# Kernel optimization log

Measured on AMD Instinct MI355X. Metric: run time of the kernel, lower is better.

Reference implementation:

```python
import jax, jax.numpy as jnp
import numpy as np

L, B, D, H = 512, 128, 512, 1024  # length, batch, input_dim, hidden


def setup_inputs() -> dict:
    key = jax.random.key(0)
    ks = jax.random.split(key, 5)
    s_in = 1.0 / np.sqrt(D + H)
    return {
        "x": jax.random.normal(ks[0], (L, B, D), dtype=jnp.float32),
        "h0": jax.random.normal(ks[1], (B, H), dtype=jnp.float32),
        "W_z": jax.random.normal(ks[2], (H, D + H), dtype=jnp.float32) * s_in,
        "b_z": jnp.zeros((H,), dtype=jnp.float32),
        "W_r": jax.random.normal(ks[3], (H, D + H), dtype=jnp.float32) * s_in,
        "b_r": jnp.zeros((H,), dtype=jnp.float32),
        "W_h": jax.random.normal(ks[4], (H, D + H), dtype=jnp.float32) * s_in,
        "b_h": jnp.zeros((H,), dtype=jnp.float32),
    }


def reference(x, h0, W_z, b_z, W_r, b_r, W_h, b_h):
    # GRU recurrence: gates computed from concat([h, x]) as in the torch code.
    def step(h, x_t):
        hx = jnp.concatenate([h, x_t], axis=-1)            # [B, H+D]
        z = jax.nn.sigmoid(hx @ W_z.T + b_z)               # update gate
        r = jax.nn.sigmoid(hx @ W_r.T + b_r)               # reset gate
        rhx = jnp.concatenate([r * h, x_t], axis=-1)       # [B, H+D]
        h_tilde = jnp.tanh(rhx @ W_h.T + b_h)
        h_new = (1.0 - z) * h + z * h_tilde
        return h_new, h_new

    _, outputs = jax.lax.scan(step, h0, x)  # outputs: [L, B, H]
    return outputs
```

## Files before the change

kernel.cpp:

```cpp
#include <hip/hip_runtime.h>
#include <cstdint>
#include <cstddef>

#define LT 512
#define BB 128
#define DD 512
#define HH 1024
#define HD 1536
#define MT (LT*BB)

typedef __bf16 bf16;
typedef __bf16 bf16x8 __attribute__((ext_vector_type(8)));
typedef __bf16 bf16x4 __attribute__((ext_vector_type(4)));
typedef float  f32x4  __attribute__((ext_vector_type(4)));

#define O_WZR 0u
#define O_WHR 6291456u
#define O_WXH 8388608u
#define O_XB  9437184u
#define O_HB  76546048u
#define O_RHB 76808192u
#define O_ZB  77070336u
#define O_BAR 77594624u
#define O_FLG 77660160u
#define WS_NEED 77922304u

#define WAIT_VM0() asm volatile("s_waitcnt vmcnt(0)" ::: "memory")
#define SCHED0()   __builtin_amdgcn_sched_barrier(0)
#define L1_INV()   asm volatile("buffer_inv sc0" ::: "memory")

template<int L> __device__ __forceinline__ f32x4 ld16s(const void* p) {
  f32x4 r;
  if constexpr (L) asm volatile("global_load_dwordx4 %0, %1, off sc0"     : "=&v"(r) : "v"(p) : "memory");
  else             asm volatile("global_load_dwordx4 %0, %1, off sc0 sc1" : "=&v"(r) : "v"(p) : "memory");
  return r;
}
template<int L> __device__ __forceinline__ float ld4s(const void* p) {
  float r;
  if constexpr (L) asm volatile("global_load_dword %0, %1, off sc0"     : "=&v"(r) : "v"(p) : "memory");
  else             asm volatile("global_load_dword %0, %1, off sc0 sc1" : "=&v"(r) : "v"(p) : "memory");
  return r;
}
template<int L> __device__ __forceinline__ unsigned ld2s(const void* p) {
  unsigned r;
  if constexpr (L) asm volatile("global_load_ushort %0, %1, off sc0"     : "=&v"(r) : "v"(p) : "memory");
  else             asm volatile("global_load_ushort %0, %1, off sc0 sc1" : "=&v"(r) : "v"(p) : "memory");
  return r;
}
template<int L> __device__ __forceinline__ void st4s(float* p, float v) {
  if constexpr (L) asm volatile("global_store_dword %0, %1, off sc0"     :: "v"(p), "v"(v) : "memory");
  else             asm volatile("global_store_dword %0, %1, off sc0 sc1" :: "v"(p), "v"(v) : "memory");
}
template<int L> __device__ __forceinline__ void st2s(bf16* p, unsigned v) {
  if constexpr (L) asm volatile("global_store_short %0, %1, off sc0"     :: "v"(p), "v"(v) : "memory");
  else             asm volatile("global_store_short %0, %1, off sc0 sc1" :: "v"(p), "v"(v) : "memory");
}
__device__ __forceinline__ void st_flag(unsigned char* p, unsigned v) {
  asm volatile("global_store_byte %0, %1, off sc0" :: "v"(p), "v"(v) : "memory");
}
__device__ __forceinline__ unsigned ld_flag(const unsigned char* p) {
  unsigned r;
  asm volatile("global_load_ubyte %0, %1, off sc0\n\ts_waitcnt vmcnt(0)"
               : "=&v"(r) : "v"(p) : "memory");
  return r;
}
__device__ __forceinline__ unsigned bf16_bits(float f) {
  bf16 b = (bf16)f;
  return (unsigned)__builtin_bit_cast(unsigned short, b);
}
__device__ __forceinline__ float bits_to_f32(unsigned u16) {
  return __builtin_bit_cast(float, u16 << 16);
}

__device__ __forceinline__ void bar_sync(unsigned* cntA, unsigned char* flagst,
                                         int t, int voteok, int& use_local,
                                         unsigned tgtA, int tid, int lane, int wv, int sb) {
  WAIT_VM0();
  __syncthreads();
  if (tid == 0)
    __hip_atomic_fetch_add(cntA, 1u, __ATOMIC_RELAXED, __HIP_MEMORY_SCOPE_AGENT);
  if (wv == 0) {
    if (tid == 0 && voteok) st_flag(flagst + sb, 1u);
    int done = 0;
    if (use_local && t >= 2) {
      int gd = 1500;
      while (gd--) {
        L1_INV();
        unsigned ok = 1u;
        if (lane < 32) ok = ld_flag(flagst + lane);
        if (__ballot(ok != 0u) == ~0ull) { done = 1; break; }
      }
      if (!done) use_local = 0;
    }
    if (!done && tid == 0) {
      int gd = 60000;
      while (__hip_atomic_load(cntA, __ATOMIC_RELAXED, __HIP_MEMORY_SCOPE_AGENT) < tgtA
             && --gd) __builtin_amdgcn_s_sleep(2);
    }
    L1_INV();
  }
  __syncthreads();
}

__global__ void k_cvt(const float* __restrict__ s, bf16* __restrict__ d, int n8) {
  int i = blockIdx.x*256 + threadIdx.x;
  if (i >= n8) return;
  const float4* p = (const float4*)s + (size_t)i*2;
  float4 a = p[0], b = p[1];
  bf16x8 v = {(bf16)a.x,(bf16)a.y,(bf16)a.z,(bf16)a.w,(bf16)b.x,(bf16)b.y,(bf16)b.z,(bf16)b.w};
  *((bf16x8*)d + i) = v;
}

__global__ void k_split_wh(const float* __restrict__ Wh, bf16* __restrict__ whr, bf16* __restrict__ wxh) {
  int i = blockIdx.x*256 + threadIdx.x;
  if (i >= 1024*192) return;
  int row = i / 192, c8 = (i % 192)*8;
  const float4* p = (const float4*)(Wh + (size_t)row*HD + c8);
  float4 a = p[0], b = p[1];
  bf16x8 v = {(bf16)a.x,(bf16)a.y,(bf16)a.z,(bf16)a.w,(bf16)b.x,(bf16)b.y,(bf16)b.z,(bf16)b.w};
  bf16* dptr = (c8 < HH) ? (whr + (size_t)row*HH + c8) : (wxh + (size_t)row*DD + (c8 - HH));
  *(bf16x8*)dptr = v;
}

__global__ void k_init_h(const float* __restrict__ h0, bf16* __restrict__ hb) {
  int i = blockIdx.x*256 + threadIdx.x;
  float4 a = ((const float4*)h0)[i];
  bf16x4 v = {(bf16)a.x,(bf16)a.y,(bf16)a.z,(bf16)a.w};
  *((bf16x4*)hb + i) = v;
}

__global__ __launch_bounds__(256) void k_gemm_xh(
    const bf16* __restrict__ xb, const bf16* __restrict__ wxh,
    const float* __restrict__ bh, float* __restrict__ out)
{
  __shared__ char As[16384];
  __shared__ char Bs[16384];
  const int bid = blockIdx.x;
  const int nt8 = bid & 7, mtb = bid >> 3;
  const int tid = threadIdx.x;
  const int lane = tid & 63, wv = tid >> 6;
  const int l15 = lane & 15, q = lane >> 4;
  const int wm = wv >> 1, wn = wv & 1;
  f32x4 acc[4][4] = {};
  const char* Ab = (const char*)(xb + (size_t)mtb*128*DD);
  const char* Bb = (const char*)(wxh + (size_t)nt8*128*DD);
  const int crow = tid >> 3, ccb = (tid & 7)*16;
  const int cdst = crow*128 + (ccb ^ ((crow & 7) << 4));
  for (int kt = 0; kt < 8; ++kt) {
    __syncthreads();
    #pragma unroll
    for (int i = 0; i < 4; ++i) {
      *(uint4*)(As + cdst + i*4096) = *(const uint4*)(Ab + (size_t)(crow + i*32)*1024 + kt*128 + ccb);
      *(uint4*)(Bs + cdst + i*4096) = *(const uint4*)(Bb + (size_t)(crow + i*32)*1024 + kt*128 + ccb);
    }
    __syncthreads();
    #pragma unroll
    for (int ks = 0; ks < 2; ++ks) {
      bf16x8 af[4], bfr[4];
      #pragma unroll
      for (int m4 = 0; m4 < 4; ++m4) {
        int row = wm*64 + m4*16 + l15, cb = ks*64 + 16*q;
        af[m4] = *(const bf16x8*)(As + row*128 + (cb ^ ((row&7)<<4)));
      }
      #pragma unroll
      for (int n4 = 0; n4 < 4; ++n4) {
        int row = wn*64 + n4*16 + l15, cb = ks*64 + 16*q;
        bfr[n4] = *(const bf16x8*)(Bs + row*128 + (cb ^ ((row&7)<<4)));
      }
      #pragma unroll
      for (int m4 = 0; m4 < 4; ++m4)
        #pragma unroll
        for (int n4 = 0; n4 < 4; ++n4)
          acc[m4][n4] = __builtin_amdgcn_mfma_f32_16x16x32_bf16(af[m4], bfr[n4], acc[m4][n4], 0, 0, 0);
    }
  }
  const int jb = nt8*128 + wn*64;
  const size_t mb = (size_t)mtb*128 + wm*64;
  #pragma unroll
  for (int n4 = 0; n4 < 4; ++n4) {
    int j = jb + n4*16 + l15;
    float bias = bh[j];
    #pragma unroll
    for (int m4 = 0; m4 < 4; ++m4)
      #pragma unroll
      for (int e = 0; e < 4; ++e) {
        size_t m = mb + m4*16 + 4*q + e;
        out[m*HH + j] = acc[m4][n4][e] + bias;
      }
  }
}

struct Frags { bf16x8 zr[4][2]; bf16x8 h[8]; };

template<int L>
__device__ __forceinline__ void tloop(const Frags& F, char* ldsW, char* scr,
    const bf16* __restrict__ xb, float* __restrict__ out,
    bf16* __restrict__ hb, bf16* __restrict__ rhb, float* __restrict__ zbuf,
    unsigned* cnt1A, unsigned* cnt2A, unsigned char* flg1, unsigned char* flg2,
    int voteok, int g, int sb, int ch, int kh, int tid, int lane, int wv,
    const float (&bias)[2], float (&hreg)[4])
{
  const int l15 = lane & 15, q = lane >> 4;
  const bf16* hrow = hb  + (size_t)(g*16 + l15)*HH;
  const bf16* rrow = rhb + (size_t)(g*16 + l15)*HH;
  const int kh384 = kh*384, kh256 = kh*256;
  const int jown = sb*32 + ch*16 + l15;
  int use_local = L ? voteok : 0;

  for (int t = 0; t < LT; ++t) {
    {
      f32x4 ab[12];
      const bf16* xrow = xb + (size_t)(t*BB + g*16 + l15)*DD;
      #pragma unroll
      for (int kk = 0; kk < 12; ++kk) {
        int kabs = kh384 + kk*32;
        if (kabs < HH) ab[kk] = ld16s<L>(hrow + kabs + 8*q);
        else           ab[kk] = *(const f32x4*)(xrow + (kabs - HH) + 8*q);
      }
      unsigned hv[2][4];
      if (sb >= 16 && kh == 0) {
        #pragma unroll
        for (int nt = 0; nt < 2; ++nt) {
          int cr = sb*64 - HH + ch*32 + nt*16 + l15;
          #pragma unroll
          for (int e = 0; e < 4; ++e)
            hv[nt][e] = ld2s<L>(hb + (size_t)(g*16 + 4*q + e)*HH + cr);
        }
      }
      WAIT_VM0(); SCHED0();
      f32x4 a0 = {}, a1 = {};
      #pragma unroll
      for (int kk = 0; kk < 12; ++kk) {
        bf16x8 a = __builtin_bit_cast(bf16x8, ab[kk]);
        bf16x8 b0, b1;
        if (kk < 8) {
          b0 = *(const bf16x8*)(ldsW + (ch*32      + l15)*2064 + kh*512 + kk*64 + 16*q);
          b1 = *(const bf16x8*)(ldsW + (ch*32 + 16 + l15)*2064 + kh*512 + kk*64 + 16*q);
        } else { b0 = F.zr[kk-8][0]; b1 = F.zr[kk-8][1]; }
        a0 = __builtin_amdgcn_mfma_f32_16x16x32_bf16(a, b0, a0, 0, 0, 0);
        a1 = __builtin_amdgcn_mfma_f32_16x16x32_bf16(a, b1, a1, 0, 0, 0);
      }
      if (kh) {
        int s = ((kh-1)*2 + ch)*2;
        *(f32x4*)(scr + (s+0)*1024 + lane*16) = a0;
        *(f32x4*)(scr + (s+1)*1024 + lane*16) = a1;
      }
      __syncthreads();
      if (kh == 0) {
        #pragma unroll
        for (int k2 = 0; k2 < 3; ++k2) {
          int s = (k2*2 + ch)*2;
          a0 += *(const f32x4*)(scr + (s+0)*1024 + lane*16);
          a1 += *(const f32x4*)(scr + (s+1)*1024 + lane*16);
        }
        if (sb < 16) {
          #pragma unroll
          for (int nt = 0; nt < 2; ++nt) {
            f32x4 ac = nt ? a1 : a0;
            int c = sb*64 + ch*32 + nt*16 + l15;
            #pragma unroll
            for (int e = 0; e < 4; ++e) {
              int m = g*16 + 4*q + e;
              float gate = 1.f/(1.f + __expf(-(ac[e] + bias[nt])));
              st4s<L>(zbuf + (size_t)m*HH + c, gate);
            }
          }
        } else {
          #pragma unroll
          for (int nt = 0; nt < 2; ++nt) {
            f32x4 ac = nt ? a1 : a0;
            int cr = sb*64 - HH + ch*32 + nt*16 + l15;
            #pragma unroll
            for (int e = 0; e < 4; ++e) {
              int m = g*16 + 4*q + e;
              float gate = 1.f/(1.f + __expf(-(ac[e] + bias[nt])));
              st2s<L>(rhb + (size_t)m*HH + cr, bf16_bits(gate * bits_to_f32(hv[nt][e])));
            }
          }
        }
      }
    }
    bar_sync(cnt1A, flg1 + t*32, t, L ? voteok : 0, use_local,
             32u*(unsigned)(t+1), tid, lane, wv, sb);
    {
      f32x4 rb[8];
      #pragma unroll
      for (int kk = 0; kk < 8; ++kk)
        rb[kk] = ld16s<L>(rrow + kh256 + kk*32 + 8*q);
      float zv[4], xh[4];
      if (kh == 0) {
        #pragma unroll
        for (int e = 0; e < 4; ++e) {
          int m = g*16 + 4*q + e;
          zv[e] = ld4s<L>(zbuf + (size_t)m*HH + jown);
          xh[e] = out[(size_t)t*(BB*HH) + (size_t)m*HH + jown];
        }
      }
      WAIT_VM0(); SCHED0();
      f32x4 acc = {};
      #pragma unroll
      for (int kk = 0; kk < 8; ++kk)
        acc = __builtin_amdgcn_mfma_f32_16x16x32_bf16(
            __builtin_bit_cast(bf16x8, rb[kk]), F.h[kk], acc, 0, 0, 0);
      if (kh) *(f32x4*)(scr + ((kh-1)*2 + ch)*1024 + lane*16) = acc;
      __syncthreads();
      if (kh == 0) {
        #pragma unroll
        for (int k2 = 0; k2 < 3; ++k2)
          acc += *(const f32x4*)(scr + (k2*2 + ch)*1024 + lane*16);
        #pragma unroll
        for (int e = 0; e < 4; ++e) {
          int m = g*16 + 4*q + e;
          size_t idx = (size_t)m*HH + jown;
          size_t oidx = (size_t)t*(BB*HH) + idx;
          float ht = tanhf(acc[e] + xh[e]);
          float hn = hreg[e] + zv[e]*(ht - hreg[e]);
          out[oidx] = hn;
          hreg[e] = hn;
          st2s<L>(hb + idx, bf16_bits(hn));
        }
      }
    }
    bar_sync(cnt2A, flg2 + t*32, t, L ? voteok : 0, use_local,
             32u*(unsigned)(t+1), tid, lane, wv, sb);
    if (L && tid == 0 && voteok && t + 2 < LT) {
      st_flag(flg1 + (t+2)*32 + sb, 0u);
      st_flag(flg2 + (t+2)*32 + sb, 0u);
    }
  }
}

__global__ __launch_bounds__(512) void k_gru(
    const bf16* __restrict__ Wzr, const bf16* __restrict__ Whr,
    const bf16* __restrict__ xb, const float* __restrict__ h0,
    const float* __restrict__ bz, const float* __restrict__ br,
    float* __restrict__ out,
    bf16* __restrict__ hb, bf16* __restrict__ rhb, float* __restrict__ zbuf,
    unsigned* __restrict__ bar, unsigned char* __restrict__ flg)
{
  extern __shared__ char smem[];
  char* ldsW = smem;
  char* scr  = smem + 132096;
  volatile int* modep = (volatile int*)(smem + 144384);

  const int tid = threadIdx.x, bid = blockIdx.x;
  const int lane = tid & 63, wv = tid >> 6;
  const int l15 = lane & 15, q = lane >> 4;
  const int g = bid & 7, sb = bid >> 3;
  const int ch = wv & 1, kh = wv >> 1;
  unsigned* grp   = bar + (size_t)g*2048;
  unsigned* cnt1A = grp + 40;
  unsigned* cnt2A = grp + 48;
  unsigned char* flg1 = flg + (size_t)g*32768;
  unsigned char* flg2 = flg + (size_t)g*32768 + 16384;

  #pragma unroll
  for (int i = 0; i < 16; ++i) {
    int ci = tid + i*512;
    int row = ci >> 7, c = ci & 127;
    int le = c*8, khs = le >> 8, rem = le & 255;
    *(uint4*)(ldsW + row*2064 + c*16) =
      *(const uint4*)(Wzr + (size_t)(sb*64 + row)*HD + khs*384 + rem);
  }
  Frags F;
  #pragma unroll
  for (int i = 0; i < 4; ++i)
    #pragma unroll
    for (int nt = 0; nt < 2; ++nt)
      F.zr[i][nt] = *(const bf16x8*)(Wzr + (size_t)(sb*64 + ch*32 + nt*16 + l15)*HD
                                     + kh*384 + (8+i)*32 + 8*q);
  #pragma unroll
  for (int kk = 0; kk < 8; ++kk)
    F.h[kk] = *(const bf16x8*)(Whr + (size_t)(sb*32 + ch*16 + l15)*HH + kh*256 + kk*32 + 8*q);

  float bias[2];
  #pragma unroll
  for (int nt = 0; nt < 2; ++nt) {
    int c = sb*64 + ch*32 + nt*16 + l15;
    bias[nt] = (sb < 16) ? bz[c] : br[c - HH];
  }
  float hreg[4];
  const int jown = sb*32 + ch*16 + l15;
  #pragma unroll
  for (int e = 0; e < 4; ++e)
    hreg[e] = h0[(size_t)(g*16 + 4*q + e)*HH + jown];

  if (tid == 0) {
    int xcc;
    asm("s_getreg_b32 %0, hwreg(HW_REG_XCC_ID)" : "=s"(xcc));
    __hip_atomic_store(&grp[sb], (unsigned)(xcc + 1), __ATOMIC_RELAXED, __HIP_MEMORY_SCOPE_AGENT);
    unsigned first = 0; int ok = 1;
    long budget = 200000;
    for (int i = 0; i < 32; ++i) {
      unsigned v = 0;
      while (budget > 0) {
        v = __hip_atomic_load(&grp[i], __ATOMIC_RELAXED, __HIP_MEMORY_SCOPE_AGENT);
        if (v) break;
        --budget; __builtin_amdgcn_s_sleep(8);
      }
      if (!v) { ok = 0; break; }
      if (i == 0) first = v;
      else if (v != first) { ok = 0; break; }
    }
    *modep = ok;
  }
  __syncthreads();
  int voteok = *modep;

  if (voteok) tloop<1>(F, ldsW, scr, xb, out, hb, rhb, zbuf, cnt1A, cnt2A,
                       flg1, flg2, 1, g, sb, ch, kh, tid, lane, wv, bias, hreg);
  else        tloop<0>(F, ldsW, scr, xb, out, hb, rhb, zbuf, cnt1A, cnt2A,
                       flg1, flg2, 0, g, sb, ch, kh, tid, lane, wv, bias, hreg);
}

extern "C" void kernel_launch(void* const* d_in, const int* in_sizes, int n_in,
                              void* d_out, int out_size, void* d_ws, size_t ws_size,
                              hipStream_t stream) {
  const float* x  = (const float*)d_in[0];
  const float* h0 = (const float*)d_in[1];
  const float* Wz = (const float*)d_in[2];
  const float* bz = (const float*)d_in[3];
  const float* Wr = (const float*)d_in[4];
  const float* br = (const float*)d_in[5];
  const float* Wh = (const float*)d_in[6];
  const float* bh = (const float*)d_in[7];
  float* out = (float*)d_out;
  char* ws = (char*)d_ws;
  if (ws_size < (size_t)WS_NEED) return;

  bf16*  wzr  = (bf16*) (ws + O_WZR);
  bf16*  whr  = (bf16*) (ws + O_WHR);
  bf16*  wxh  = (bf16*) (ws + O_WXH);
  bf16*  xbb  = (bf16*) (ws + O_XB);
  bf16*  hb   = (bf16*) (ws + O_HB);
  bf16*  rhb  = (bf16*) (ws + O_RHB);
  float* zbuf = (float*)(ws + O_ZB);
  unsigned* bar = (unsigned*)(ws + O_BAR);
  unsigned char* flg = (unsigned char*)(ws + O_FLG);

  hipMemsetAsync(bar, 0, 65536, stream);
  k_cvt<<<16384, 256, 0, stream>>>(x, xbb, MT*DD/8);
  k_cvt<<<768, 256, 0, stream>>>(Wz, wzr, HH*HD/8);
  k_cvt<<<768, 256, 0, stream>>>(Wr, wzr + (size_t)HH*HD, HH*HD/8);
  k_split_wh<<<768, 256, 0, stream>>>(Wh, whr, wxh);
  k_init_h<<<128, 256, 0, stream>>>(h0, hb);
  k_gemm_xh<<<4096, 256, 0, stream>>>(xbb, wxh, bh, out);

  hipFuncSetAttribute((const void*)k_gru, hipFuncAttributeMaxDynamicSharedMemorySize, 144400);
  k_gru<<<256, 512, 144400, stream>>>(wzr, whr, xbb, h0, bz, br, out, hb, rhb, zbuf, bar, flg);
}
```

Measured before the change: 5.241 ms.

## Streamline grid barrier to single-wave signaling and prefetch next-step x and out

Removes the full-block bar_sync, which waited on all memory ops and ran two __syncthreads. Only the kh==0 waves now store results, and a wave-to-wave LDS handshake lets a single wave do the cross-block atomic and flag polling before one __syncthreads. The x operand for step t+1 is prefetched during the second phase, and the xh loads from out are moved earlier so they overlap the first GEMM, with partial vmcnt waits. Risks include subtle ordering bugs in the LDS spin handshake and extra register pressure from keeping ab live across iterations. Launch bounds also change to (512,2).

After: 6.155 ms. 17.4% more time.

```diff
diff --git a/kernel.cpp b/kernel.cpp
--- a/kernel.cpp
+++ b/kernel.cpp
@@ -25,9 +25,11 @@
 #define O_FLG 77660160u
 #define WS_NEED 77922304u
 
-#define WAIT_VM0() asm volatile("s_waitcnt vmcnt(0)" ::: "memory")
-#define SCHED0()   __builtin_amdgcn_sched_barrier(0)
-#define L1_INV()   asm volatile("buffer_inv sc0" ::: "memory")
+#define WAIT_VM0()  asm volatile("s_waitcnt vmcnt(0)" ::: "memory")
+#define WAIT_VM4()  asm volatile("s_waitcnt vmcnt(4)" ::: "memory")
+#define WAIT_VM12() asm volatile("s_waitcnt vmcnt(12)" ::: "memory")
+#define SCHED0()    __builtin_amdgcn_sched_barrier(0)
+#define L1_INV()    asm volatile("buffer_inv sc0" ::: "memory")
 
 template<int L> __device__ __forceinline__ f32x4 ld16s(const void* p) {
   f32x4 r;
@@ -55,6 +57,16 @@
   if constexpr (L) asm volatile("global_store_short %0, %1, off sc0"     :: "v"(p), "v"(v) : "memory");
   else             asm volatile("global_store_short %0, %1, off sc0 sc1" :: "v"(p), "v"(v) : "memory");
 }
+__device__ __forceinline__ f32x4 ld16p(const void* p) {
+  f32x4 r;
+  asm volatile("global_load_dwordx4 %0, %1, off" : "=&v"(r) : "v"(p) : "memory");
+  return r;
+}
+__device__ __forceinline__ float ld4p(const void* p) {
+  float r;
+  asm volatile("global_load_dword %0, %1, off" : "=&v"(r) : "v"(p) : "memory");
+  return r;
+}
 __device__ __forceinline__ void st_flag(unsigned char* p, unsigned v) {
   asm volatile("global_store_byte %0, %1, off sc0" :: "v"(p), "v"(v) : "memory");
 }
@@ -70,36 +82,6 @@
 }
 __device__ __forceinline__ float bits_to_f32(unsigned u16) {
   return __builtin_bit_cast(float, u16 << 16);
-}
-
-__device__ __forceinline__ void bar_sync(unsigned* cntA, unsigned char* flagst,
-                                         int t, int voteok, int& use_local,
-                                         unsigned tgtA, int tid, int lane, int wv, int sb) {
-  WAIT_VM0();
-  __syncthreads();
-  if (tid == 0)
-    __hip_atomic_fetch_add(cntA, 1u, __ATOMIC_RELAXED, __HIP_MEMORY_SCOPE_AGENT);
-  if (wv == 0) {
-    if (tid == 0 && voteok) st_flag(flagst + sb, 1u);
-    int done = 0;
-    if (use_local && t >= 2) {
-      int gd = 1500;
-      while (gd--) {
-        L1_INV();
-        unsigned ok = 1u;
-        if (lane < 32) ok = ld_flag(flagst + lane);
-        if (__ballot(ok != 0u) == ~0ull) { done = 1; break; }
-      }
-      if (!done) use_local = 0;
-    }
-    if (!done && tid == 0) {
-      int gd = 60000;
-      while (__hip_atomic_load(cntA, __ATOMIC_RELAXED, __HIP_MEMORY_SCOPE_AGENT) < tgtA
-             && --gd) __builtin_amdgcn_s_sleep(2);
-    }
-    L1_INV();
-  }
-  __syncthreads();
 }
 
 __global__ void k_cvt(const float* __restrict__ s, bf16* __restrict__ d, int n8) {
@@ -200,22 +182,32 @@
     int voteok, int g, int sb, int ch, int kh, int tid, int lane, int wv,
     const float (&bias)[2], float (&hreg)[4])
 {
+  __shared__ unsigned s_done[2];
   const int l15 = lane & 15, q = lane >> 4;
   const bf16* hrow = hb  + (size_t)(g*16 + l15)*HH;
   const bf16* rrow = rhb + (size_t)(g*16 + l15)*HH;
   const int kh384 = kh*384, kh256 = kh*256;
   const int jown = sb*32 + ch*16 + l15;
   int use_local = L ? voteok : 0;
+  if (tid == 0) { s_done[0] = 0; s_done[1] = 0; }
+
+  f32x4 ab[12];
+  {
+    const bf16* xrow0 = xb + (size_t)(g*16 + l15)*DD;
+    #pragma unroll
+    for (int kk = 0; kk < 12; ++kk) {
+      int kabs = kh384 + kk*32;
+      if (kabs >= HH) ab[kk] = ld16p(xrow0 + (kabs - HH) + 8*q);
+    }
+  }
 
   for (int t = 0; t < LT; ++t) {
+    float xh[4];
     {
-      f32x4 ab[12];
-      const bf16* xrow = xb + (size_t)(t*BB + g*16 + l15)*DD;
       #pragma unroll
       for (int kk = 0; kk < 12; ++kk) {
         int kabs = kh384 + kk*32;
         if (kabs < HH) ab[kk] = ld16s<L>(hrow + kabs + 8*q);
-        else           ab[kk] = *(const f32x4*)(xrow + (kabs - HH) + 8*q);
       }
       unsigned hv[2][4];
       if (sb >= 16 && kh == 0) {
@@ -227,7 +219,13 @@
             hv[nt][e] = ld2s<L>(hb + (size_t)(g*16 + 4*q + e)*HH + cr);
         }
       }
-      WAIT_VM0(); SCHED0();
+      if (kh == 0) {
+        #pragma unroll
+        for (int e = 0; e < 4; ++e)
+          xh[e] = ld4p(out + (size_t)t*(BB*HH) + (size_t)(g*16 + 4*q + e)*HH + jown);
+      }
+      if (kh == 0) { WAIT_VM4(); } else { WAIT_VM0(); }
+      SCHED0();
       f32x4 a0 = {}, a1 = {};
       #pragma unroll
       for (int kk = 0; kk < 12; ++kk) {
@@ -278,25 +276,65 @@
             }
           }
         }
-      }
+        WAIT_VM0();
+        if (ch == 1) {
+          if (lane == 0)
+            __hip_atomic_fetch_add(&s_done[0], 1u, __ATOMIC_RELAXED, __HIP_MEMORY_SCOPE_WORKGROUP);
+        } else {
+          if (lane == 0) {
+            int gd = 1<<22;
+            while (!__hip_atomic_load(&s_done[0], __ATOMIC_RELAXED, __HIP_MEMORY_SCOPE_WORKGROUP) && --gd) {}
+            __hip_atomic_store(&s_done[0], 0u, __ATOMIC_RELAXED, __HIP_MEMORY_SCOPE_WORKGROUP);
+            __hip_atomic_fetch_add(cnt1A, 1u, __ATOMIC_RELAXED, __HIP_MEMORY_SCOPE_AGENT);
+            if (L && voteok) st_flag(flg1 + t*32 + sb, 1u);
+          }
+          int done = 0;
+          if (use_local && t >= 2) {
+            int gd = 1500;
+            while (gd--) {
+              L1_INV();
+              unsigned ok = 1u;
+              if (lane < 32) ok = ld_flag(flg1 + t*32 + lane);
+              if (__ballot(ok != 0u) == ~0ull) { done = 1; break; }
+            }
+            if (!done) use_local = 0;
+          }
+          if (!done && lane == 0) {
+            unsigned tgt = 32u*(unsigned)(t+1);
+            int gd = 60000;
+            while (__hip_atomic_load(cnt1A, __ATOMIC_RELAXED, __HIP_MEMORY_SCOPE_AGENT) < tgt
+                   && --gd) __builtin_amdgcn_s_sleep(2);
+          }
+          L1_INV();
+        }
+      }
+      __syncthreads();
     }
-    bar_sync(cnt1A, flg1 + t*32, t, L ? voteok : 0, use_local,
-             32u*(unsigned)(t+1), tid, lane, wv, sb);
     {
       f32x4 rb[8];
       #pragma unroll
       for (int kk = 0; kk < 8; ++kk)
         rb[kk] = ld16s<L>(rrow + kh256 + kk*32 + 8*q);
-      float zv[4], xh[4];
+      float zv[4];
       if (kh == 0) {
         #pragma unroll
-        for (int e = 0; e < 4; ++e) {
-          int m = g*16 + 4*q + e;
-          zv[e] = ld4s<L>(zbuf + (size_t)m*HH + jown);
-          xh[e] = out[(size_t)t*(BB*HH) + (size_t)m*HH + jown];
-        }
-      }
-      WAIT_VM0(); SCHED0();
+        for (int e = 0; e < 4; ++e)
+          zv[e] = ld4s<L>(zbuf + (size_t)(g*16 + 4*q + e)*HH + jown);
+      }
+      {
+        int tn = (t+1 < LT) ? t+1 : t;
+        const bf16* xrow_n = xb + (size_t)(tn*BB + g*16 + l15)*DD;
+        #pragma unroll
+        for (int kk = 0; kk < 12; ++kk) {
+          int kabs = kh384 + kk*32;
+          if (kabs >= HH) ab[kk] = ld16p(xrow_n + (kabs - HH) + 8*q);
+        }
+      }
+      if      (kh == 3) { WAIT_VM12(); }
+      else if (kh == 2) { WAIT_VM4(); }
+      else if (kh == 0) { WAIT_VM4(); }
+      else              { WAIT_VM0(); }
+      SCHED0();
       f32x4 acc = {};
       #pragma unroll
       for (int kk = 0; kk < 8; ++kk)
@@ -305,6 +343,7 @@
       if (kh) *(f32x4*)(scr + ((kh-1)*2 + ch)*1024 + lane*16) = acc;
       __syncthreads();
       if (kh == 0) {
+        WAIT_VM0(); SCHED0();
         #pragma unroll
         for (int k2 = 0; k2 < 3; ++k2)
           acc += *(const f32x4*)(scr + (k2*2 + ch)*1024 + lane*16);
@@ -319,18 +358,48 @@
           hreg[e] = hn;
           st2s<L>(hb + idx, bf16_bits(hn));
         }
+        WAIT_VM0();
+        if (ch == 1) {
+          if (lane == 0)
+            __hip_atomic_fetch_add(&s_done[1], 1u, __ATOMIC_RELAXED, __HIP_MEMORY_SCOPE_WORKGROUP);
+        } else {
+          if (lane == 0) {
+            int gd = 1<<22;
+            while (!__hip_atomic_load(&s_done[1], __ATOMIC_RELAXED, __HIP_MEMORY_SCOPE_WORKGROUP) && --gd) {}
+            __hip_atomic_store(&s_done[1], 0u, __ATOMIC_RELAXED, __HIP_MEMORY_SCOPE_WORKGROUP);
+            __hip_atomic_fetch_add(cnt2A, 1u, __ATOMIC_RELAXED, __HIP_MEMORY_SCOPE_AGENT);
+            if (L && voteok) st_flag(flg2 + t*32 + sb, 1u);
+          }
+          int done = 0;
+          if (use_local && t >= 2) {
+            int gd = 1500;
+            while (gd--) {
+              L1_INV();
+              unsigned ok = 1u;
+              if (lane < 32) ok = ld_flag(flg2 + t*32 + lane);
+              if (__ballot(ok != 0u) == ~0ull) { done = 1; break; }
+            }
+            if (!done) use_local = 0;
+          }
+          if (!done && lane == 0) {
+            unsigned tgt = 32u*(unsigned)(t+1);
+            int gd = 60000;
+            while (__hip_atomic_load(cnt2A, __ATOMIC_RELAXED, __HIP_MEMORY_SCOPE_AGENT) < tgt
+                   && --gd) __builtin_amdgcn_s_sleep(2);
+          }
+          L1_INV();
+        }
+      }
+      __syncthreads();
+      if (L && tid == 0 && voteok && t + 2 < LT) {
+        st_flag(flg1 + (t+2)*32 + sb, 0u);
+        st_flag(flg2 + (t+2)*32 + sb, 0u);
       }
     }
-    bar_sync(cnt2A, flg2 + t*32, t, L ? voteok : 0, use_local,
-             32u*(unsigned)(t+1), tid, lane, wv, sb);
-    if (L && tid == 0 && voteok && t + 2 < LT) {
-      st_flag(flg1 + (t+2)*32 + sb, 0u);
-      st_flag(flg2 + (t+2)*32 + sb, 0u);
-    }
-  }
-}
-
-__global__ __launch_bounds__(512) void k_gru(
+  }
+}
+
+__global__ __launch_bounds__(512, 2) void k_gru(
     const bf16* __restrict__ Wzr, const bf16* __restrict__ Whr,
     const bf16* __restrict__ xb, const float* __restrict__ h0,
     const float* __restrict__ bz, const float* __restrict__ br,
@@ -341,7 +410,7 @@
   extern __shared__ char smem[];
   char* ldsW = smem;
   char* scr  = smem + 132096;
-  volatile int* modep = (volatile int*)(smem + 144384);
+  __shared__ int s_mode;
 
   const int tid = threadIdx.x, bid = blockIdx.x;
   const int lane = tid & 63, wv = tid >> 6;
@@ -402,10 +471,10 @@
       if (i == 0) first = v;
       else if (v != first) { ok = 0; break; }
     }
-    *modep = ok;
+    s_mode = ok;
   }
   __syncthreads();
-  int voteok = *modep;
+  int voteok = s_mode;
 
   if (voteok) tloop<1>(F, ldsW, scr, xb, out, hb, rhb, zbuf, cnt1A, cnt2A,
                        flg1, flg2, 1, g, sb, ch, kh, tid, lane, wv, bias, hreg);
@@ -446,6 +515,6 @@
   k_init_h<<<128, 256, 0, stream>>>(h0, hb);
   k_gemm_xh<<<4096, 256, 0, stream>>>(xbb, wxh, bh, out);
 
-  hipFuncSetAttribute((const void*)k_gru, hipFuncAttributeMaxDynamicSharedMemorySize, 144400);
-  k_gru<<<256, 512, 144400, stream>>>(wzr, whr, xbb, h0, bz, br, out, hb, rhb, zbuf, bar, flg);
-}
+  hipFuncSetAttribute((const void*)k_gru, hipFuncAttributeMaxDynamicSharedMemorySize, 144384);
+  k_gru<<<256, 512, 144384, stream>>>(wzr, whr, xbb, h0, bz, br, out, hb, rhb, zbuf, bar, flg);
+}
```

## Co-locate z and r gate columns per block to keep z gate in LDS

Applied to the files above, without the earlier changes.

Each block used to compute 64 columns that were either all z-gate or all r-gate, so the z gate went out to a global buffer and was read back after the grid barrier. Now each block computes the 32 z columns and the 32 r columns that match its own hidden slice. The z values stay in shared memory and are read by the same block in phase two. This removes a global store and a global load per step on the serial critical path, at the cost of a little more LDS and a changed weight-row mapping.

Result: faster. 4.616 ms (-11.9%).

```diff
diff --git a/kernel.cpp b/kernel.cpp
--- a/kernel.cpp
+++ b/kernel.cpp
@@ -20,7 +20,6 @@
 #define O_XB  9437184u
 #define O_HB  76546048u
 #define O_RHB 76808192u
-#define O_ZB  77070336u
 #define O_BAR 77594624u
 #define O_FLG 77660160u
 #define WS_NEED 77922304u
@@ -35,21 +34,11 @@
   else             asm volatile("global_load_dwordx4 %0, %1, off sc0 sc1" : "=&v"(r) : "v"(p) : "memory");
   return r;
 }
-template<int L> __device__ __forceinline__ float ld4s(const void* p) {
-  float r;
-  if constexpr (L) asm volatile("global_load_dword %0, %1, off sc0"     : "=&v"(r) : "v"(p) : "memory");
-  else             asm volatile("global_load_dword %0, %1, off sc0 sc1" : "=&v"(r) : "v"(p) : "memory");
-  return r;
-}
 template<int L> __device__ __forceinline__ unsigned ld2s(const void* p) {
   unsigned r;
   if constexpr (L) asm volatile("global_load_ushort %0, %1, off sc0"     : "=&v"(r) : "v"(p) : "memory");
   else             asm volatile("global_load_ushort %0, %1, off sc0 sc1" : "=&v"(r) : "v"(p) : "memory");
   return r;
-}
-template<int L> __device__ __forceinline__ void st4s(float* p, float v) {
-  if constexpr (L) asm volatile("global_store_dword %0, %1, off sc0"     :: "v"(p), "v"(v) : "memory");
-  else             asm volatile("global_store_dword %0, %1, off sc0 sc1" :: "v"(p), "v"(v) : "memory");
 }
 template<int L> __device__ __forceinline__ void st2s(bf16* p, unsigned v) {
   if constexpr (L) asm volatile("global_store_short %0, %1, off sc0"     :: "v"(p), "v"(v) : "memory");
@@ -193,9 +182,9 @@
 struct Frags { bf16x8 zr[4][2]; bf16x8 h[8]; };
 
 template<int L>
-__device__ __forceinline__ void tloop(const Frags& F, char* ldsW, char* scr,
+__device__ __forceinline__ void tloop(const Frags& F, char* ldsW, char* scr, float* zsL,
     const bf16* __restrict__ xb, float* __restrict__ out,
-    bf16* __restrict__ hb, bf16* __restrict__ rhb, float* __restrict__ zbuf,
+    bf16* __restrict__ hb, bf16* __restrict__ rhb,
     unsigned* cnt1A, unsigned* cnt2A, unsigned char* flg1, unsigned char* flg2,
     int voteok, int g, int sb, int ch, int kh, int tid, int lane, int wv,
     const float (&bias)[2], float (&hreg)[4])
@@ -218,10 +207,10 @@
         else           ab[kk] = *(const f32x4*)(xrow + (kabs - HH) + 8*q);
       }
       unsigned hv[2][4];
-      if (sb >= 16 && kh == 0) {
+      if (ch == 1 && kh == 0) {
         #pragma unroll
         for (int nt = 0; nt < 2; ++nt) {
-          int cr = sb*64 - HH + ch*32 + nt*16 + l15;
+          int cr = sb*32 + nt*16 + l15;
           #pragma unroll
           for (int e = 0; e < 4; ++e)
             hv[nt][e] = ld2s<L>(hb + (size_t)(g*16 + 4*q + e)*HH + cr);
@@ -253,23 +242,20 @@
           a0 += *(const f32x4*)(scr + (s+0)*1024 + lane*16);
           a1 += *(const f32x4*)(scr + (s+1)*1024 + lane*16);
         }
-        if (sb < 16) {
+        if (ch == 0) {
           #pragma unroll
           for (int nt = 0; nt < 2; ++nt) {
             f32x4 ac = nt ? a1 : a0;
-            int c = sb*64 + ch*32 + nt*16 + l15;
             #pragma unroll
-            for (int e = 0; e < 4; ++e) {
-              int m = g*16 + 4*q + e;
-              float gate = 1.f/(1.f + __expf(-(ac[e] + bias[nt])));
-              st4s<L>(zbuf + (size_t)m*HH + c, gate);
-            }
+            for (int e = 0; e < 4; ++e)
+              zsL[(nt*16 + l15)*16 + 4*q + e] =
+                1.f/(1.f + __expf(-(ac[e] + bias[nt])));
           }
         } else {
           #pragma unroll
           for (int nt = 0; nt < 2; ++nt) {
             f32x4 ac = nt ? a1 : a0;
-            int cr = sb*64 - HH + ch*32 + nt*16 + l15;
+            int cr = sb*32 + nt*16 + l15;
             #pragma unroll
             for (int e = 0; e < 4; ++e) {
               int m = g*16 + 4*q + e;
@@ -287,14 +273,11 @@
       #pragma unroll
       for (int kk = 0; kk < 8; ++kk)
         rb[kk] = ld16s<L>(rrow + kh256 + kk*32 + 8*q);
-      float zv[4], xh[4];
+      float xh[4];
       if (kh == 0) {
         #pragma unroll
-        for (int e = 0; e < 4; ++e) {
-          int m = g*16 + 4*q + e;
-          zv[e] = ld4s<L>(zbuf + (size_t)m*HH + jown);
-          xh[e] = out[(size_t)t*(BB*HH) + (size_t)m*HH + jown];
-        }
+        for (int e = 0; e < 4; ++e)
+          xh[e] = out[(size_t)t*(BB*HH) + (size_t)(g*16 + 4*q + e)*HH + jown];
       }
       WAIT_VM0(); SCHED0();
       f32x4 acc = {};
@@ -308,6 +291,7 @@
         #pragma unroll
         for (int k2 = 0; k2 < 3; ++k2)
           acc += *(const f32x4*)(scr + (k2*2 + ch)*1024 + lane*16);
+        f32x4 zv = *(const f32x4*)(zsL + (ch*16 + l15)*16 + 4*q);
         #pragma unroll
         for (int e = 0; e < 4; ++e) {
           int m = g*16 + 4*q + e;
@@ -335,13 +319,14 @@
     const bf16* __restrict__ xb, const float* __restrict__ h0,
     const float* __restrict__ bz, const float* __restrict__ br,
     float* __restrict__ out,
-    bf16* __restrict__ hb, bf16* __restrict__ rhb, float* __restrict__ zbuf,
+    bf16* __restrict__ hb, bf16* __restrict__ rhb,
     unsigned* __restrict__ bar, unsigned char* __restrict__ flg)
 {
   extern __shared__ char smem[];
-  char* ldsW = smem;
-  char* scr  = smem + 132096;
-  volatile int* modep = (volatile int*)(smem + 144384);
+  char*  ldsW = smem;
+  char*  scr  = smem + 132096;
+  float* zsL  = (float*)(smem + 144384);
+  volatile int* modep = (volatile int*)(smem + 146432);
 
   const int tid = threadIdx.x, bid = blockIdx.x;
   const int lane = tid & 63, wv = tid >> 6;
@@ -359,16 +344,18 @@
     int ci = tid + i*512;
     int row = ci >> 7, c = ci & 127;
     int le = c*8, khs = le >> 8, rem = le & 255;
+    int gr = (row < 32) ? sb*32 + row : HH + sb*32 + (row - 32);
     *(uint4*)(ldsW + row*2064 + c*16) =
-      *(const uint4*)(Wzr + (size_t)(sb*64 + row)*HD + khs*384 + rem);
+      *(const uint4*)(Wzr + (size_t)gr*HD + khs*384 + rem);
   }
   Frags F;
   #pragma unroll
   for (int i = 0; i < 4; ++i)
     #pragma unroll
     for (int nt = 0; nt < 2; ++nt)
-      F.zr[i][nt] = *(const bf16x8*)(Wzr + (size_t)(sb*64 + ch*32 + nt*16 + l15)*HD
-                                     + kh*384 + (8+i)*32 + 8*q);
+      F.zr[i][nt] = *(const bf16x8*)(Wzr
+          + (size_t)((ch ? HH : 0) + sb*32 + nt*16 + l15)*HD
+          + kh*384 + (8+i)*32 + 8*q);
   #pragma unroll
   for (int kk = 0; kk < 8; ++kk)
     F.h[kk] = *(const bf16x8*)(Whr + (size_t)(sb*32 + ch*16 + l15)*HH + kh*256 + kk*32 + 8*q);
@@ -376,8 +363,8 @@
   float bias[2];
   #pragma unroll
   for (int nt = 0; nt < 2; ++nt) {
-    int c = sb*64 + ch*32 + nt*16 + l15;
-    bias[nt] = (sb < 16) ? bz[c] : br[c - HH];
+    int c = sb*32 + nt*16 + l15;
+    bias[nt] = (ch == 0) ? bz[c] : br[c];
   }
   float hreg[4];
   const int jown = sb*32 + ch*16 + l15;
@@ -407,9 +394,9 @@
   __syncthreads();
   int voteok = *modep;
 
-  if (voteok) tloop<1>(F, ldsW, scr, xb, out, hb, rhb, zbuf, cnt1A, cnt2A,
+  if (voteok) tloop<1>(F, ldsW, scr, zsL, xb, out, hb, rhb, cnt1A, cnt2A,
                        flg1, flg2, 1, g, sb, ch, kh, tid, lane, wv, bias, hreg);
-  else        tloop<0>(F, ldsW, scr, xb, out, hb, rhb, zbuf, cnt1A, cnt2A,
+  else        tloop<0>(F, ldsW, scr, zsL, xb, out, hb, rhb, cnt1A, cnt2A,
                        flg1, flg2, 0, g, sb, ch, kh, tid, lane, wv, bias, hreg);
 }
 
@@ -434,7 +421,6 @@
   bf16*  xbb  = (bf16*) (ws + O_XB);
   bf16*  hb   = (bf16*) (ws + O_HB);
   bf16*  rhb  = (bf16*) (ws + O_RHB);
-  float* zbuf = (float*)(ws + O_ZB);
   unsigned* bar = (unsigned*)(ws + O_BAR);
   unsigned char* flg = (unsigned char*)(ws + O_FLG);
 
@@ -446,6 +432,6 @@
   k_init_h<<<128, 256, 0, stream>>>(h0, hb);
   k_gemm_xh<<<4096, 256, 0, stream>>>(xbb, wxh, bh, out);
 
-  hipFuncSetAttribute((const void*)k_gru, hipFuncAttributeMaxDynamicSharedMemorySize, 144400);
-  k_gru<<<256, 512, 144400, stream>>>(wzr, whr, xbb, h0, bz, br, out, hb, rhb, zbuf, bar, flg);
-}
+  hipFuncSetAttribute((const void*)k_gru, hipFuncAttributeMaxDynamicSharedMemorySize, 146448);
+  k_gru<<<256, 512, 146448, stream>>>(wzr, whr, xbb, h0, bz, br, out, hb, rhb, bar, flg);
+}
```
